# Kernel tuning notes

Hardware: AMD Instinct MI355X
Metric: run time of the kernel (lower is better)

## Reference

```python
import jax, jax.numpy as jnp
import numpy as np

B, L, M, F = 64, 1024, 256, 256


def setup_inputs() -> dict:
    key = jax.random.key(0)
    k1, k2 = jax.random.split(key)
    patch_features = jax.random.normal(k1, (B, L, F), dtype=jnp.float32)
    queue = jax.random.normal(k2, (L, M, F), dtype=jnp.float32)
    return {"patch_features": patch_features, "queue": queue}


def reference(patch_features, queue):
    # sim[b, l, m] = <patch_features[b, l], queue[l, m]>  (batched per-location matmul)
    sim = jnp.einsum('blf,lmf->blm', patch_features, queue)
    # original takes topk(5) then keeps only index 0 == argmax over memory slots
    idx = jnp.argmax(sim, axis=-1)                      # [B, L]
    # N[b, l] = queue[l, idx[b, l]]
    N = queue[jnp.arange(queue.shape[0])[None, :], idx]  # [B, L, F]
    return N
```

## Files before the change

### kernel.cpp

```cpp
#include <hip/hip_runtime.h>

#define B_ 64
#define L_ 1024
#define M_ 256
#define F_ 256

typedef __attribute__((ext_vector_type(8))) short short8;
typedef __attribute__((ext_vector_type(16))) float f32x16;
typedef unsigned int u32;

struct Frag3 { short8 h, m, l; };

__device__ __forceinline__ u32 asu(float f) { union { float f; u32 u; } c; c.f = f; return c.u; }
__device__ __forceinline__ float asf(u32 u) { union { float f; u32 u; } c; c.u = u; return c.f; }
__device__ __forceinline__ u32 pack2(u32 lo, u32 hi) {
    return __builtin_amdgcn_perm(hi, lo, 0x07060302u);
}
__device__ __forceinline__ float4 ld4(const float* p) {
    return *reinterpret_cast<const float4*>(p);
}

__device__ __forceinline__ void async_cp16(const float* g, float* l) {
    __builtin_amdgcn_global_load_lds(
        (const __attribute__((address_space(1))) u32*)g,
        (__attribute__((address_space(3))) u32*)l,
        16, 0, 0);
}

__device__ __forceinline__ Frag3 split8(float4 a, float4 b) {
    float x[8] = {a.x, a.y, a.z, a.w, b.x, b.y, b.z, b.w};
    u32 xb[8], rb[8], sb[8];
#pragma unroll
    for (int e = 0; e < 8; ++e) {
        xb[e] = asu(x[e]);
        float hf = asf(xb[e] & 0xFFFF0000u);
        float r  = x[e] - hf;
        rb[e] = asu(r);
        float mf = asf(rb[e] & 0xFFFF0000u);
        float r2 = r - mf;
        sb[e] = asu(r2);
    }
    union { u32 w[4]; short8 s; } H, M, Lo;
#pragma unroll
    for (int d = 0; d < 4; ++d) {
        H.w[d]  = pack2(xb[2 * d], xb[2 * d + 1]);
        M.w[d]  = pack2(rb[2 * d], rb[2 * d + 1]);
        Lo.w[d] = pack2(sb[2 * d], sb[2 * d + 1]);
    }
    Frag3 f; f.h = H.s; f.m = M.s; f.l = Lo.s; return f;
}

#define MFMA6(ACC, A, Bf)                                                        \
    ACC = __builtin_amdgcn_mfma_f32_32x32x16_bf16((A).m, (Bf).m, ACC, 0, 0, 0);  \
    ACC = __builtin_amdgcn_mfma_f32_32x32x16_bf16((A).h, (Bf).l, ACC, 0, 0, 0);  \
    ACC = __builtin_amdgcn_mfma_f32_32x32x16_bf16((A).l, (Bf).h, ACC, 0, 0, 0);  \
    ACC = __builtin_amdgcn_mfma_f32_32x32x16_bf16((A).h, (Bf).m, ACC, 0, 0, 0);  \
    ACC = __builtin_amdgcn_mfma_f32_32x32x16_bf16((A).m, (Bf).h, ACC, 0, 0, 0);  \
    ACC = __builtin_amdgcn_mfma_f32_32x32x16_bf16((A).h, (Bf).h, ACC, 0, 0, 0)

__launch_bounds__(256, 2)
__global__ void mq_mfma_sb4_kernel(const float* __restrict__ patch,
                                   const float* __restrict__ queue,
                                   float* __restrict__ out) {
    const int l    = blockIdx.x;
    const int t    = threadIdx.x;
    const int lane = t & 63;
    const int w    = t >> 6;
    const int bt   = w & 1;
    const int mtg  = w >> 1;
    const int r32  = lane & 31;
    const int kh   = lane >> 5;

    __shared__ __align__(16) float Ql[256 * 32];
    __shared__ __align__(16) float Pl[64 * 32];

    const int lrow = lane >> 3;
    const int lcol = lane & 7;
    const float* qsrcw = queue + ((size_t)l * M_ + w * 64 + lrow) * F_ + (lcol ^ lrow) * 4;
    const float* psrcw = patch + ((size_t)(w * 16 + lrow) * L_ + l) * F_ + (lcol ^ lrow) * 4;

    f32x16 acc[4];
#pragma unroll
    for (int mt = 0; mt < 4; ++mt) acc[mt] = (f32x16)0.f;

    const int s7 = r32 & 7;
    const int ra = bt * 32 + r32;

#pragma unroll 1
    for (int ft = 0; ft < 8; ++ft) {
        __builtin_amdgcn_s_barrier();
        __builtin_amdgcn_sched_barrier(0);
        {
            const int o = ft * 32;
#pragma unroll
            for (int k = 0; k < 8; ++k)
                async_cp16(qsrcw + (size_t)k * 8 * F_ + o, &Ql[(w * 8 + k) * 256]);
#pragma unroll
            for (int k = 0; k < 2; ++k)
                async_cp16(psrcw + (size_t)k * 8 * L_ * F_ + o, &Pl[(w * 2 + k) * 256]);
        }
        asm volatile("s_waitcnt vmcnt(0)" ::: "memory");
        __builtin_amdgcn_sched_barrier(0);
        __builtin_amdgcn_s_barrier();
        __builtin_amdgcn_sched_barrier(0);

#pragma unroll
        for (int kk = 0; kk < 2; ++kk) {
            const int c0 = kk * 4 + kh * 2;
            const float4 a0 = ld4(&Pl[ra * 32 + ((c0 ^ s7) * 4)]);
            const float4 a1 = ld4(&Pl[ra * 32 + (((c0 + 1) ^ s7) * 4)]);
            const Frag3 A = split8(a0, a1);
#pragma unroll
            for (int mt = 0; mt < 4; ++mt) {
                const int rb = mtg * 128 + mt * 32 + r32;
                const float4 b0 = ld4(&Ql[rb * 32 + ((c0 ^ s7) * 4)]);
                const float4 b1 = ld4(&Ql[rb * 32 + (((c0 + 1) ^ s7) * 4)]);
                const Frag3 Bf = split8(b0, b1);
                MFMA6(acc[mt], A, Bf);
            }
        }
    }

    __syncthreads();

    float* pval = (float*)&Pl[0];
    int*   pidx = (int*)&Pl[0] + 128;
    int*   sidx = (int*)&Pl[0] + 256;
#pragma unroll
    for (int r = 0; r < 16; ++r) {
        float bv = acc[0][r];
        int   bi = mtg * 128 + r32;
#pragma unroll
        for (int mt = 1; mt < 4; ++mt) {
            const float cv = acc[mt][r];
            const int   ci = mtg * 128 + mt * 32 + r32;
            if (cv > bv) { bv = cv; bi = ci; }
        }
#pragma unroll
        for (int off = 16; off >= 1; off >>= 1) {
            const float ov = __shfl_xor(bv, off);
            const int   oi = __shfl_xor(bi, off);
            if (ov > bv || (ov == bv && oi < bi)) { bv = ov; bi = oi; }
        }
        if (r32 == 0) {
            const int b = bt * 32 + (r & 3) + 8 * (r >> 2) + 4 * kh;
            pval[mtg * 64 + b] = bv;
            pidx[mtg * 64 + b] = bi;
        }
    }
    __syncthreads();

    if (t < 64) {
        const float v0 = pval[t], v1 = pval[64 + t];
        sidx[t] = (v1 > v0) ? pidx[64 + t] : pidx[t];
    }
    __syncthreads();

    const int cb = t >> 6;
    const int cc = t & 63;
#pragma unroll
    for (int b0 = 0; b0 < 64; b0 += 4) {
        const int b  = b0 + cb;
        const int mi = sidx[b];
        const float4 v = ld4(&queue[((size_t)l * M_ + mi) * F_ + cc * 4]);
        *reinterpret_cast<float4*>(&out[((size_t)b * L_ + l) * F_ + cc * 4]) = v;
    }
}

extern "C" void kernel_launch(void* const* d_in, const int* in_sizes, int n_in,
                              void* d_out, int out_size, void* d_ws, size_t ws_size,
                              hipStream_t stream) {
    const float* patch = (const float*)d_in[0];
    const float* queue = (const float*)d_in[1];
    float* out = (float*)d_out;
    mq_mfma_sb4_kernel<<<dim3(L_), dim3(256), 0, stream>>>(patch, queue, out);
}
```

Baseline: 106.7 us.

## Retile warps into square 64x64 output tiles to cut operand reloads and splits

Each warp previously owned a 32-row batch strip times 128 memory slots, loading and splitting one A fragment and four B fragments per k-step. Now each warp owns a 64x64 tile (both batch halves times its own 64 slots), loading and splitting two A and two B fragments per k-step. This cuts LDS reads and bf16 split work per MFMA. The argmax reduction now merges four partial results per batch row instead of two. Launch bounds drop the min-blocks hint, which may change register allocation and occupancy.

```diff
diff --git a/kernel.cpp b/kernel.cpp
--- a/kernel.cpp
+++ b/kernel.cpp
@@ -58,16 +58,14 @@
     ACC = __builtin_amdgcn_mfma_f32_32x32x16_bf16((A).m, (Bf).h, ACC, 0, 0, 0);  \
     ACC = __builtin_amdgcn_mfma_f32_32x32x16_bf16((A).h, (Bf).h, ACC, 0, 0, 0)
 
-__launch_bounds__(256, 2)
-__global__ void mq_mfma_sb4_kernel(const float* __restrict__ patch,
-                                   const float* __restrict__ queue,
-                                   float* __restrict__ out) {
+__launch_bounds__(256)
+__global__ void mq_mfma_sq_kernel(const float* __restrict__ patch,
+                                  const float* __restrict__ queue,
+                                  float* __restrict__ out) {
     const int l    = blockIdx.x;
     const int t    = threadIdx.x;
     const int lane = t & 63;
     const int w    = t >> 6;
-    const int bt   = w & 1;
-    const int mtg  = w >> 1;
     const int r32  = lane & 31;
     const int kh   = lane >> 5;
 
@@ -79,12 +77,14 @@
     const float* qsrcw = queue + ((size_t)l * M_ + w * 64 + lrow) * F_ + (lcol ^ lrow) * 4;
     const float* psrcw = patch + ((size_t)(w * 16 + lrow) * L_ + l) * F_ + (lcol ^ lrow) * 4;
 
-    f32x16 acc[4];
-#pragma unroll
-    for (int mt = 0; mt < 4; ++mt) acc[mt] = (f32x16)0.f;
-
-    const int s7 = r32 & 7;
-    const int ra = bt * 32 + r32;
+    f32x16 acc00 = (f32x16)0.f, acc01 = (f32x16)0.f;
+    f32x16 acc10 = (f32x16)0.f, acc11 = (f32x16)0.f;
+
+    const int s7  = r32 & 7;
+    const int ra0 = r32;
+    const int ra1 = 32 + r32;
+    const int rb0 = (w * 2) * 32 + r32;
+    const int rb1 = (w * 2 + 1) * 32 + r32;
 
 #pragma unroll 1
     for (int ft = 0; ft < 8; ++ft) {
@@ -107,16 +107,21 @@
 #pragma unroll
         for (int kk = 0; kk < 2; ++kk) {
             const int c0 = kk * 4 + kh * 2;
-            const float4 a0 = ld4(&Pl[ra * 32 + ((c0 ^ s7) * 4)]);
-            const float4 a1 = ld4(&Pl[ra * 32 + (((c0 + 1) ^ s7) * 4)]);
-            const Frag3 A = split8(a0, a1);
-#pragma unroll
-            for (int mt = 0; mt < 4; ++mt) {
-                const int rb = mtg * 128 + mt * 32 + r32;
-                const float4 b0 = ld4(&Ql[rb * 32 + ((c0 ^ s7) * 4)]);
-                const float4 b1 = ld4(&Ql[rb * 32 + (((c0 + 1) ^ s7) * 4)]);
-                const Frag3 Bf = split8(b0, b1);
-                MFMA6(acc[mt], A, Bf);
+            const Frag3 A0 = split8(ld4(&Pl[ra0 * 32 + ((c0 ^ s7) * 4)]),
+                                    ld4(&Pl[ra0 * 32 + (((c0 + 1) ^ s7) * 4)]));
+            const Frag3 A1 = split8(ld4(&Pl[ra1 * 32 + ((c0 ^ s7) * 4)]),
+                                    ld4(&Pl[ra1 * 32 + (((c0 + 1) ^ s7) * 4)]));
+            {
+                const Frag3 Bf = split8(ld4(&Ql[rb0 * 32 + ((c0 ^ s7) * 4)]),
+                                        ld4(&Ql[rb0 * 32 + (((c0 + 1) ^ s7) * 4)]));
+                MFMA6(acc00, A0, Bf);
+                MFMA6(acc10, A1, Bf);
+            }
+            {
+                const Frag3 Bf = split8(ld4(&Ql[rb1 * 32 + ((c0 ^ s7) * 4)]),
+                                        ld4(&Ql[rb1 * 32 + (((c0 + 1) ^ s7) * 4)]));
+                MFMA6(acc01, A0, Bf);
+                MFMA6(acc11, A1, Bf);
             }
         }
     }
@@ -124,35 +129,55 @@
     __syncthreads();
 
     float* pval = (float*)&Pl[0];
-    int*   pidx = (int*)&Pl[0] + 128;
-    int*   sidx = (int*)&Pl[0] + 256;
+    int*   pidx = (int*)&Pl[0] + 256;
+    int*   sidx = (int*)&Pl[0] + 512;
 #pragma unroll
     for (int r = 0; r < 16; ++r) {
-        float bv = acc[0][r];
-        int   bi = mtg * 128 + r32;
-#pragma unroll
-        for (int mt = 1; mt < 4; ++mt) {
-            const float cv = acc[mt][r];
-            const int   ci = mtg * 128 + mt * 32 + r32;
-            if (cv > bv) { bv = cv; bi = ci; }
-        }
-#pragma unroll
-        for (int off = 16; off >= 1; off >>= 1) {
-            const float ov = __shfl_xor(bv, off);
-            const int   oi = __shfl_xor(bi, off);
-            if (ov > bv || (ov == bv && oi < bi)) { bv = ov; bi = oi; }
-        }
-        if (r32 == 0) {
-            const int b = bt * 32 + (r & 3) + 8 * (r >> 2) + 4 * kh;
-            pval[mtg * 64 + b] = bv;
-            pidx[mtg * 64 + b] = bi;
+        const int crow = (r & 3) + 8 * (r >> 2) + 4 * kh;
+        {
+            float bv = acc00[r];
+            int   bi = w * 64 + r32;
+            {
+                const float cv = acc01[r];
+                const int   ci = w * 64 + 32 + r32;
+                if (cv > bv) { bv = cv; bi = ci; }
+            }
+#pragma unroll
+            for (int off = 16; off >= 1; off >>= 1) {
+                const float ov = __shfl_xor(bv, off);
+                const int   oi = __shfl_xor(bi, off);
+                if (ov > bv || (ov == bv && oi < bi)) { bv = ov; bi = oi; }
+            }
+            if (r32 == 0) { pval[w * 64 + crow] = bv; pidx[w * 64 + crow] = bi; }
+        }
+        {
+            float bv = acc10[r];
+            int   bi = w * 64 + r32;
+            {
+                const float cv = acc11[r];
+                const int   ci = w * 64 + 32 + r32;
+                if (cv > bv) { bv = cv; bi = ci; }
+            }
+#pragma unroll
+            for (int off = 16; off >= 1; off >>= 1) {
+                const float ov = __shfl_xor(bv, off);
+                const int   oi = __shfl_xor(bi, off);
+                if (ov > bv || (ov == bv && oi < bi)) { bv = ov; bi = oi; }
+            }
+            if (r32 == 0) { pval[w * 64 + 32 + crow] = bv; pidx[w * 64 + 32 + crow] = bi; }
         }
     }
     __syncthreads();
 
     if (t < 64) {
-        const float v0 = pval[t], v1 = pval[64 + t];
-        sidx[t] = (v1 > v0) ? pidx[64 + t] : pidx[t];
+        float bv = pval[t];
+        int   bi = pidx[t];
+#pragma unroll
+        for (int g = 1; g < 4; ++g) {
+            const float cv = pval[g * 64 + t];
+            if (cv > bv) { bv = cv; bi = pidx[g * 64 + t]; }
+        }
+        sidx[t] = bi;
     }
     __syncthreads();
 
@@ -173,5 +198,5 @@
     const float* patch = (const float*)d_in[0];
     const float* queue = (const float*)d_in[1];
     float* out = (float*)d_out;
-    mq_mfma_sb4_kernel<<<dim3(L_), dim3(256), 0, stream>>>(patch, queue, out);
-}
+    mq_mfma_sq_kernel<<<dim3(L_), dim3(256), 0, stream>>>(patch, queue, out);
+}
```

Measured after the change: 119.9 us. 1.12x slower.
